# Optimization experiments

Measured on AMD Instinct MI355X. Metric: run time of the kernel, lower is better.

The kernel has to match this reference:

```python
import jax, jax.numpy as jnp
import numpy as np

N, F, M, B = 100000, 256, 10, 32768
DECAY = 0.9


def setup_inputs() -> dict:
    key = jax.random.key(0)
    ks = jax.random.split(key, 16)
    s = 1.0 / np.sqrt(F)
    # forward args
    node_indices = jax.random.permutation(ks[0], N)[:B]  # unique indices
    node_features = jax.random.normal(ks[1], (B, F), jnp.float32)
    # per-node state
    hidden_states = jax.random.normal(ks[2], (N, F), jnp.float32) * 0.1
    cell_states = jax.random.normal(ks[3], (N, F), jnp.float32) * 0.1
    temporal_memory = jax.random.normal(ks[4], (N, M, F), jnp.float32) * 0.1
    memory_ptr = jax.random.randint(ks[5], (N,), 0, M)
    # LSTMCell params (gate order i, f, g, o as in torch)
    W_ih = jax.random.normal(ks[6], (4 * F, F), jnp.float32) * s
    W_hh = jax.random.normal(ks[7], (4 * F, F), jnp.float32) * s
    b_ih = jax.random.normal(ks[8], (4 * F,), jnp.float32) * s
    b_hh = jax.random.normal(ks[9], (4 * F,), jnp.float32) * s
    # attention read params
    Wq = jax.random.normal(ks[10], (F, F), jnp.float32) * s
    bq = jnp.zeros((F,), jnp.float32)
    Wk = jax.random.normal(ks[11], (F, F), jnp.float32) * s
    bk = jnp.zeros((F,), jnp.float32)
    Wv = jax.random.normal(ks[12], (F, F), jnp.float32) * s
    bv = jnp.zeros((F,), jnp.float32)
    return dict(node_indices=node_indices, node_features=node_features,
                hidden_states=hidden_states, cell_states=cell_states,
                temporal_memory=temporal_memory, memory_ptr=memory_ptr,
                W_ih=W_ih, W_hh=W_hh, b_ih=b_ih, b_hh=b_hh,
                Wq=Wq, bq=bq, Wk=Wk, bk=bk, Wv=Wv, bv=bv)


def reference(node_indices, node_features, hidden_states, cell_states,
              temporal_memory, memory_ptr, W_ih, W_hh, b_ih, b_hh,
              Wq, bq, Wk, bk, Wv, bv):
    idx = node_indices
    feat = node_features.shape[-1]
    # --- update_memory: LSTMCell on gathered per-node states ---
    h_prev = hidden_states[idx]              # (B, F)
    c_prev = cell_states[idx]                # (B, F)
    gates = node_features @ W_ih.T + b_ih + h_prev @ W_hh.T + b_hh
    i, f, g, o = jnp.split(gates, 4, axis=-1)
    c_new = jax.nn.sigmoid(f) * c_prev + jax.nn.sigmoid(i) * jnp.tanh(g)
    h_new = jax.nn.sigmoid(o) * jnp.tanh(c_new)
    # --- scatter into circular temporal memory + decay previous slot ---
    ptr = memory_ptr[idx]                    # (B,)
    tm = temporal_memory.at[idx, ptr].set(node_features)
    prev = ptr - 1                           # -1 wraps; decay only applied if ptr > 0
    old = tm[idx, prev]                      # (B, F)
    tm = tm.at[idx, prev].set(jnp.where((ptr > 0)[:, None], old * DECAY, old))
    # --- get_temporal_context: gather + tiny attention over M slots ---
    mem = tm[idx]                            # (B, M, F)
    q = h_new @ Wq.T + bq                    # (B, F)  hidden_states[idx] post-update == h_new
    k = mem @ Wk.T + bk                      # (B, M, F)
    v = mem @ Wv.T + bv                      # (B, M, F)
    scores = jnp.einsum('bf,bmf->bm', q, k) / jnp.sqrt(jnp.asarray(feat, q.dtype))
    w = jax.nn.softmax(scores, axis=-1)      # (B, M)
    context = jnp.einsum('bmf,bm->bf', v, w) # (B, F)
    return context
```

## Files before the change

kernel.cpp:

```cpp
#include <hip/hip_runtime.h>
#include <hip/hip_bf16.h>

constexpr int NB = 32768;
constexpr int NF = 256;
constexpr int NM = 10;
constexpr float DECAY = 0.9f;

using bf16x8 = __attribute__((ext_vector_type(8))) short;
using f32x4  = __attribute__((ext_vector_type(4))) float;

static __device__ __forceinline__ ushort f2bf(float x) {
    unsigned u = __float_as_uint(x);
    unsigned r = (u + 0x7fffu + ((u >> 16) & 1u)) >> 16;
    return (ushort)r;
}
static __device__ __forceinline__ float bf2f(ushort x) {
    return __uint_as_float(((unsigned)x) << 16);
}
static __device__ __forceinline__ float sigmoid_f(float x) {
    return 1.f / (1.f + __expf(-x));
}
static __device__ __forceinline__ float tanh_f(float x) {
    float e = __expf(2.f * x);
    return (e - 1.f) / (e + 1.f);
}
static __device__ __forceinline__ void gload16(const void* g, void* l) {
    __builtin_amdgcn_global_load_lds(
        (const __attribute__((address_space(1))) unsigned int*)g,
        (__attribute__((address_space(3))) unsigned int*)l, 16, 0, 0);
}

constexpr int PB_ACAT = 16384;
constexpr int PB_WGI  = PB_ACAT + 1024;
constexpr int PB_WQKT = PB_WGI + 256;
constexpr int PB_WV   = PB_WQKT + 256;
constexpr int PB_TOT  = PB_WV + 1;

__global__ __launch_bounds__(256) void k_prep(
    const float* __restrict__ W_ih, const float* __restrict__ W_hh,
    const float* __restrict__ b_ih, const float* __restrict__ b_hh,
    const float* __restrict__ Wq, const float* __restrict__ bq,
    const float* __restrict__ Wk, const float* __restrict__ Wv,
    const float* __restrict__ nf, const float* __restrict__ hidden,
    const int* __restrict__ idx,
    ushort* __restrict__ Wgi, float* __restrict__ bsum,
    ushort* __restrict__ WqkT, float* __restrict__ bqk,
    ushort* __restrict__ Wvb, ushort* __restrict__ Acat)
{
    const int blk = blockIdx.x, tid = threadIdx.x;
    if (blk < PB_ACAT) {
        int t = blk * 256 + tid;
        int row = t >> 7;
        int c4 = (t & 127) * 4;
        const float* src = (c4 < 256) ? (nf + (size_t)row * 256 + c4)
                                      : (hidden + (size_t)idx[row] * 256 + (c4 - 256));
        float4 v = *reinterpret_cast<const float4*>(src);
        ushort4 o;
        o.x = f2bf(v.x); o.y = f2bf(v.y); o.z = f2bf(v.z); o.w = f2bf(v.w);
        *reinterpret_cast<ushort4*>(Acat + (size_t)row * 512 + c4) = o;
    } else if (blk < PB_WGI) {
        int j = blk - PB_ACAT;
        int f = j >> 2, g = j & 3;
        int sr = g * 256 + f;
        for (int c = tid; c < 512; c += 256) {
            float v = (c < 256) ? W_ih[sr * 256 + c] : W_hh[sr * 256 + (c - 256)];
            Wgi[j * 512 + c] = f2bf(v);
        }
        if (tid == 0) bsum[j] = b_ih[sr] + b_hh[sr];
    } else if (blk < PB_WQKT) {
        int i = blk - PB_WGI, a = tid;
        float s = 0.f;
#pragma unroll 8
        for (int j = 0; j < 256; ++j) s += Wq[j * 256 + a] * Wk[j * 256 + i];
        WqkT[i * 256 + a] = f2bf(s * 0.0625f);
    } else if (blk < PB_WV) {
        int t = (blk - PB_WQKT) * 256 + tid;
        Wvb[t] = f2bf(Wv[t]);
    } else {
        int i = tid;
        float s = 0.f;
#pragma unroll 8
        for (int j = 0; j < 256; ++j) s += bq[j] * Wk[j * 256 + i];
        bqk[i] = s * 0.0625f;
    }
}

__global__ __launch_bounds__(256) void k_gates2(
    const ushort* __restrict__ Acat, const ushort* __restrict__ Wgi,
    const float* __restrict__ bsum, const int* __restrict__ idx,
    const float* __restrict__ cell, ushort* __restrict__ h_new)
{
    __shared__ ushort As[128 * 32];
    __shared__ ushort Bs[128 * 32];
    const int t = threadIdx.x;
    const int w = t >> 6, l = t & 63;
    const int wr = w >> 1, wc = w & 1;
    const int lr = l & 15, lk = l >> 4;
    const int row0 = blockIdx.x * 128;
    const int col0 = blockIdx.y * 128;

    f32x4 acc[4][4];
#pragma unroll
    for (int m = 0; m < 4; ++m)
#pragma unroll
        for (int n = 0; n < 4; ++n) acc[m][n] = f32x4{0.f, 0.f, 0.f, 0.f};

    const int srow = l >> 2;
    const int scol = (l & 3) * 8;
    const int u0 = w * 2, u1 = u0 + 1;
    const ushort* aS0 = Acat + (size_t)(row0 + u0 * 16 + srow) * 512 + scol;
    const ushort* aS1 = Acat + (size_t)(row0 + u1 * 16 + srow) * 512 + scol;
    const ushort* bS0 = Wgi  + (size_t)(col0 + u0 * 16 + srow) * 512 + scol;
    const ushort* bS1 = Wgi  + (size_t)(col0 + u1 * 16 + srow) * 512 + scol;
    ushort* aL0 = As + u0 * 512; ushort* aL1 = As + u1 * 512;
    ushort* bL0 = Bs + u0 * 512; ushort* bL1 = Bs + u1 * 512;

    for (int k0 = 0; k0 < 512; k0 += 32) {
        gload16(aS0 + k0, aL0);
        gload16(aS1 + k0, aL1);
        gload16(bS0 + k0, bL0);
        gload16(bS1 + k0, bL1);
        __syncthreads();
        bf16x8 af[4], bfr[4];
#pragma unroll
        for (int m = 0; m < 4; ++m)
            af[m] = *reinterpret_cast<const bf16x8*>(As + (wr * 64 + m * 16 + lr) * 32 + lk * 8);
#pragma unroll
        for (int n = 0; n < 4; ++n)
            bfr[n] = *reinterpret_cast<const bf16x8*>(Bs + (wc * 64 + n * 16 + lr) * 32 + lk * 8);
#pragma unroll
        for (int m = 0; m < 4; ++m)
#pragma unroll
            for (int n = 0; n < 4; ++n)
                acc[m][n] = __builtin_amdgcn_mfma_f32_16x16x32_bf16(af[m], bfr[n], acc[m][n], 0, 0, 0);
        __syncthreads();
    }

    float bb[4];
#pragma unroll
    for (int n = 0; n < 4; ++n) bb[n] = bsum[col0 + wc * 64 + n * 16 + lr];
#pragma unroll
    for (int m = 0; m < 4; ++m)
#pragma unroll
        for (int n = 0; n < 4; ++n)
#pragma unroll
            for (int r = 0; r < 4; ++r) acc[m][n][r] += bb[n];

    const int g0 = lr & 3;
    const int fq = lr >> 2;
    const bool is0 = (g0 == 0), is1 = (g0 == 1), is2 = (g0 == 2), is3 = (g0 == 3);
    const int fbase = (col0 >> 2) + wc * 16;

    int nodev[4];
#pragma unroll
    for (int r = 0; r < 4; ++r)
        nodev[r] = idx[row0 + wr * 64 + g0 * 16 + lk * 4 + r];

#pragma unroll
    for (int n = 0; n < 4; ++n) {
#pragma unroll
        for (int r = 0; r < 4; ++r) {
            float own = is0 ? acc[0][n][r] : is1 ? acc[1][n][r] : is2 ? acc[2][n][r] : acc[3][n][r];
            float s1  = is0 ? acc[1][n][r] : is1 ? acc[0][n][r] : is2 ? acc[3][n][r] : acc[2][n][r];
            float s2  = is0 ? acc[2][n][r] : is1 ? acc[3][n][r] : is2 ? acc[0][n][r] : acc[1][n][r];
            float s3  = is0 ? acc[3][n][r] : is1 ? acc[2][n][r] : is2 ? acc[1][n][r] : acc[0][n][r];
            float r1 = __shfl_xor(s1, 1, 64);
            float r2 = __shfl_xor(s2, 2, 64);
            float r3 = __shfl_xor(s3, 3, 64);
            float gi = is0 ? own : is1 ? r1 : is2 ? r2 : r3;
            float gf = is1 ? own : is0 ? r1 : is3 ? r2 : r3;
            float gg = is2 ? own : is3 ? r1 : is0 ? r2 : r3;
            float go = is3 ? own : is2 ? r1 : is1 ? r2 : r3;
            int fg = fbase + n * 4 + fq;
            float cp = cell[(size_t)nodev[r] * 256 + fg];
            float cn = sigmoid_f(gf) * cp + sigmoid_f(gi) * tanh_f(gg);
            float hn = sigmoid_f(go) * tanh_f(cn);
            int grow = row0 + wr * 64 + g0 * 16 + lk * 4 + r;
            h_new[(size_t)grow * 256 + fg] = f2bf(hn);
        }
    }
}

__global__ __launch_bounds__(256) void k_qk(
    const ushort* __restrict__ hnew, const ushort* __restrict__ WqkT,
    const float* __restrict__ bqk, ushort* __restrict__ qbuf)
{
    __shared__ ushort As[64 * 32];
    const int t = threadIdx.x, w = t >> 6, l = t & 63;
    const int lr = l & 15, lk = l >> 4;
    const int row0 = blockIdx.x * 64;

    f32x4 acc[4][4];
#pragma unroll
    for (int m = 0; m < 4; ++m)
#pragma unroll
        for (int n = 0; n < 4; ++n) acc[m][n] = f32x4{0.f, 0.f, 0.f, 0.f};

    const int srow = w * 16 + (l >> 2);
    const int scol = (l & 3) * 8;
    const ushort* aS = hnew + (size_t)(row0 + srow) * 256 + scol;
    ushort* aL = As + (w * 16) * 32;

    const ushort* bptr[4];
#pragma unroll
    for (int n = 0; n < 4; ++n) bptr[n] = WqkT + (size_t)(w * 64 + n * 16 + lr) * 256 + lk * 8;

    for (int k0 = 0; k0 < 256; k0 += 32) {
        gload16(aS + k0, aL);
        __syncthreads();
        bf16x8 a[4], b[4];
#pragma unroll
        for (int m = 0; m < 4; ++m)
            a[m] = *reinterpret_cast<const bf16x8*>(As + (m * 16 + lr) * 32 + lk * 8);
#pragma unroll
        for (int n = 0; n < 4; ++n) b[n] = *reinterpret_cast<const bf16x8*>(bptr[n] + k0);
#pragma unroll
        for (int m = 0; m < 4; ++m)
#pragma unroll
            for (int n = 0; n < 4; ++n)
                acc[m][n] = __builtin_amdgcn_mfma_f32_16x16x32_bf16(a[m], b[n], acc[m][n], 0, 0, 0);
        __syncthreads();
    }

#pragma unroll
    for (int m = 0; m < 4; ++m)
#pragma unroll
        for (int n = 0; n < 4; ++n) {
            int colc = w * 64 + n * 16 + lr;
            float bbq = bqk[colc];
#pragma unroll
            for (int r = 0; r < 4; ++r) {
                int row = row0 + m * 16 + lk * 4 + r;
                qbuf[(size_t)row * 256 + colc] = f2bf(acc[m][n][r] + bbq);
            }
        }
}

static __device__ __forceinline__ int swzb(int row, int byteInRow) {
    return (row * 512 + byteInRow) ^ ((row & 7) << 4);
}

__global__ __launch_bounds__(256) void k_attnout(
    const ushort* __restrict__ qbuf, const ushort* __restrict__ Wvb,
    const float* __restrict__ bv, const int* __restrict__ idx,
    const int* __restrict__ mptr, const float* __restrict__ tm,
    const float* __restrict__ nf, float* __restrict__ out)
{
    __shared__ ushort sQ[16 * 256];
    char* sB = (char*)sQ;
    const int t = threadIdx.x, w = t >> 6, l = t & 63;
    const int lr = l & 15, lk = l >> 4;
    const int row0 = blockIdx.x * 16;

#pragma unroll
    for (int ch = t; ch < 512; ch += 256) {
        int row = ch >> 5;
        int pos = (ch & 31) * 16;
        *reinterpret_cast<uint4*>(sB + swzb(row, pos)) =
            *reinterpret_cast<const uint4*>((const char*)(qbuf + (size_t)(row0 + row) * 256) + pos);
    }
    __syncthreads();

    {
        const int b0 = row0 + w * 4;
        int nodes[4], ptrs[4];
#pragma unroll
        for (int r = 0; r < 4; ++r) { nodes[r] = idx[b0 + r]; ptrs[r] = mptr[nodes[r]]; }

#pragma unroll
        for (int rr = 0; rr < 4; ++rr) {
            int row = w * 4 + rr;
            int b = b0 + rr;
            int node = nodes[rr];
            int ptr = ptrs[rr];
            ushort4 q4 = *(const ushort4*)(sB + swzb(row, l * 8));
            float q0 = bf2f(q4.x), q1 = bf2f(q4.y), q2 = bf2f(q4.z), q3 = bf2f(q4.w);
            const float* base = tm + (size_t)node * (NM * NF);

            float4 mem[NM];
            float sc[NM];
#pragma unroll
            for (int m = 0; m < NM; ++m) {
                float4 v;
                if (m == ptr) {
                    v = *reinterpret_cast<const float4*>(nf + (size_t)b * 256 + l * 4);
                } else {
                    v = *reinterpret_cast<const float4*>(base + (size_t)m * 256 + l * 4);
                    if (ptr > 0 && m == ptr - 1) { v.x *= DECAY; v.y *= DECAY; v.z *= DECAY; v.w *= DECAY; }
                }
                mem[m] = v;
                sc[m] = q0 * v.x + q1 * v.y + q2 * v.z + q3 * v.w;
            }
#pragma unroll
            for (int m = 0; m < NM; ++m) {
                float s = sc[m];
#pragma unroll
                for (int d = 1; d < 64; d <<= 1) s += __shfl_xor(s, d, 64);
                sc[m] = s;
            }
            float mx = sc[0];
#pragma unroll
            for (int m = 1; m < NM; ++m) mx = fmaxf(mx, sc[m]);
            float e[NM], sum = 0.f;
#pragma unroll
            for (int m = 0; m < NM; ++m) { e[m] = __expf(sc[m] - mx); sum += e[m]; }
            float inv = 1.f / sum;

            float4 c = {0.f, 0.f, 0.f, 0.f};
#pragma unroll
            for (int m = 0; m < NM; ++m) {
                float wm = e[m] * inv;
                c.x += wm * mem[m].x; c.y += wm * mem[m].y; c.z += wm * mem[m].z; c.w += wm * mem[m].w;
            }
            ushort4 o;
            o.x = f2bf(c.x); o.y = f2bf(c.y); o.z = f2bf(c.z); o.w = f2bf(c.w);
            *(ushort4*)(sB + swzb(row, l * 8)) = o;
        }
    }
    __syncthreads();

    f32x4 acc[4];
#pragma unroll
    for (int n = 0; n < 4; ++n) acc[n] = f32x4{0.f, 0.f, 0.f, 0.f};
    const ushort* vptr[4];
#pragma unroll
    for (int n = 0; n < 4; ++n) vptr[n] = Wvb + (size_t)(w * 64 + n * 16 + lr) * 256 + lk * 8;

#pragma unroll 2
    for (int k = 0; k < 256; k += 32) {
        bf16x8 a = *reinterpret_cast<const bf16x8*>(sB + swzb(lr, (k + lk * 8) * 2));
        bf16x8 b[4];
#pragma unroll
        for (int n = 0; n < 4; ++n) b[n] = *reinterpret_cast<const bf16x8*>(vptr[n] + k);
#pragma unroll
        for (int n = 0; n < 4; ++n)
            acc[n] = __builtin_amdgcn_mfma_f32_16x16x32_bf16(a, b[n], acc[n], 0, 0, 0);
    }
#pragma unroll
    for (int n = 0; n < 4; ++n) {
        int colc = w * 64 + n * 16 + lr;
        float bbv = bv[colc];
#pragma unroll
        for (int r = 0; r < 4; ++r) {
            int row = lk * 4 + r;
            out[(size_t)(row0 + row) * 256 + colc] = acc[n][r] + bbv;
        }
    }
}

extern "C" void kernel_launch(void* const* d_in, const int* in_sizes, int n_in,
                              void* d_out, int out_size, void* d_ws, size_t ws_size,
                              hipStream_t stream) {
    const int*   node_indices = (const int*)  d_in[0];
    const float* node_feats   = (const float*)d_in[1];
    const float* hidden       = (const float*)d_in[2];
    const float* cell         = (const float*)d_in[3];
    const float* tmem         = (const float*)d_in[4];
    const int*   memory_ptr   = (const int*)  d_in[5];
    const float* W_ih         = (const float*)d_in[6];
    const float* W_hh         = (const float*)d_in[7];
    const float* b_ih         = (const float*)d_in[8];
    const float* b_hh         = (const float*)d_in[9];
    const float* Wq           = (const float*)d_in[10];
    const float* bq           = (const float*)d_in[11];
    const float* Wk           = (const float*)d_in[12];
    const float* Wv           = (const float*)d_in[14];
    const float* bv           = (const float*)d_in[15];

    char* ws = (char*)d_ws;
    size_t off = 0;
    auto alloc = [&](size_t bytes) { char* p = ws + off; off += (bytes + 255) & ~(size_t)255; return p; };

    ushort* Wgi   = (ushort*)alloc((size_t)1024 * 512 * 2);
    ushort* WqkT  = (ushort*)alloc((size_t)256 * 256 * 2);
    ushort* Wvb   = (ushort*)alloc((size_t)256 * 256 * 2);
    float*  bqk   = (float*) alloc((size_t)256 * 4);
    float*  bsum  = (float*) alloc((size_t)1024 * 4);
    ushort* Acat  = (ushort*)alloc((size_t)NB * 512 * 2);
    ushort* hnew  = (ushort*)alloc((size_t)NB * 256 * 2);
    ushort* qbuf  = (ushort*)alloc((size_t)NB * 256 * 2);

    k_prep<<<PB_TOT, 256, 0, stream>>>(W_ih, W_hh, b_ih, b_hh, Wq, bq, Wk, Wv,
                                       node_feats, hidden, node_indices,
                                       Wgi, bsum, WqkT, bqk, Wvb, Acat);
    k_gates2<<<dim3(NB / 128, 8), 256, 0, stream>>>(Acat, Wgi, bsum, node_indices, cell, hnew);
    k_qk<<<NB / 64, 256, 0, stream>>>(hnew, WqkT, bqk, qbuf);
    k_attnout<<<NB / 16, 256, 0, stream>>>(qbuf, Wvb, bv, node_indices, memory_ptr,
                                           tmem, node_feats, (float*)d_out);
}
```

Measured before the change: 218.8 us.

## Double-buffer LDS tiles in GEMM kernels and read q directly from global

The gates and qk GEMM kernels now double-buffer their shared-memory A/B tiles, prefetching the next K-slice while MFMAs consume the current one. This halves the barriers per iteration and overlaps global loads with compute. The attention-output kernel drops its staging of q into swizzled LDS and loads each row's q values directly from global memory. The cost is twice the shared memory in the GEMMs, which may reduce occupancy.

```diff
diff --git a/kernel.cpp b/kernel.cpp
--- a/kernel.cpp
+++ b/kernel.cpp
@@ -90,8 +90,8 @@
     const float* __restrict__ bsum, const int* __restrict__ idx,
     const float* __restrict__ cell, ushort* __restrict__ h_new)
 {
-    __shared__ ushort As[128 * 32];
-    __shared__ ushort Bs[128 * 32];
+    __shared__ ushort As[2][128 * 32];
+    __shared__ ushort Bs[2][128 * 32];
     const int t = threadIdx.x;
     const int w = t >> 6, l = t & 63;
     const int wr = w >> 1, wc = w & 1;
@@ -112,28 +112,35 @@
     const ushort* aS1 = Acat + (size_t)(row0 + u1 * 16 + srow) * 512 + scol;
     const ushort* bS0 = Wgi  + (size_t)(col0 + u0 * 16 + srow) * 512 + scol;
     const ushort* bS1 = Wgi  + (size_t)(col0 + u1 * 16 + srow) * 512 + scol;
-    ushort* aL0 = As + u0 * 512; ushort* aL1 = As + u1 * 512;
-    ushort* bL0 = Bs + u0 * 512; ushort* bL1 = Bs + u1 * 512;
+
+    gload16(aS0, As[0] + u0 * 512);
+    gload16(aS1, As[0] + u1 * 512);
+    gload16(bS0, Bs[0] + u0 * 512);
+    gload16(bS1, Bs[0] + u1 * 512);
+    __syncthreads();
 
     for (int k0 = 0; k0 < 512; k0 += 32) {
-        gload16(aS0 + k0, aL0);
-        gload16(aS1 + k0, aL1);
-        gload16(bS0 + k0, bL0);
-        gload16(bS1 + k0, bL1);
-        __syncthreads();
+        const int cur = (k0 >> 5) & 1;
+        if (k0 + 32 < 512) {
+            const int nxt = cur ^ 1;
+            gload16(aS0 + k0 + 32, As[nxt] + u0 * 512);
+            gload16(aS1 + k0 + 32, As[nxt] + u1 * 512);
+            gload16(bS0 + k0 + 32, Bs[nxt] + u0 * 512);
+            gload16(bS1 + k0 + 32, Bs[nxt] + u1 * 512);
+        }
         bf16x8 af[4], bfr[4];
 #pragma unroll
         for (int m = 0; m < 4; ++m)
-            af[m] = *reinterpret_cast<const bf16x8*>(As + (wr * 64 + m * 16 + lr) * 32 + lk * 8);
+            af[m] = *reinterpret_cast<const bf16x8*>(As[cur] + (wr * 64 + m * 16 + lr) * 32 + lk * 8);
 #pragma unroll
         for (int n = 0; n < 4; ++n)
-            bfr[n] = *reinterpret_cast<const bf16x8*>(Bs + (wc * 64 + n * 16 + lr) * 32 + lk * 8);
+            bfr[n] = *reinterpret_cast<const bf16x8*>(Bs[cur] + (wc * 64 + n * 16 + lr) * 32 + lk * 8);
 #pragma unroll
         for (int m = 0; m < 4; ++m)
 #pragma unroll
             for (int n = 0; n < 4; ++n)
                 acc[m][n] = __builtin_amdgcn_mfma_f32_16x16x32_bf16(af[m], bfr[n], acc[m][n], 0, 0, 0);
-        __syncthreads();
+        if (k0 + 32 < 512) __syncthreads();
     }
 
     float bb[4];
@@ -185,7 +192,7 @@
     const ushort* __restrict__ hnew, const ushort* __restrict__ WqkT,
     const float* __restrict__ bqk, ushort* __restrict__ qbuf)
 {
-    __shared__ ushort As[64 * 32];
+    __shared__ ushort As[2][64 * 32];
     const int t = threadIdx.x, w = t >> 6, l = t & 63;
     const int lr = l & 15, lk = l >> 4;
     const int row0 = blockIdx.x * 64;
@@ -199,19 +206,22 @@
     const int srow = w * 16 + (l >> 2);
     const int scol = (l & 3) * 8;
     const ushort* aS = hnew + (size_t)(row0 + srow) * 256 + scol;
-    ushort* aL = As + (w * 16) * 32;
+    const int aLoff = (w * 16) * 32;
 
     const ushort* bptr[4];
 #pragma unroll
     for (int n = 0; n < 4; ++n) bptr[n] = WqkT + (size_t)(w * 64 + n * 16 + lr) * 256 + lk * 8;
 
+    gload16(aS, As[0] + aLoff);
+    __syncthreads();
+
     for (int k0 = 0; k0 < 256; k0 += 32) {
-        gload16(aS + k0, aL);
-        __syncthreads();
+        const int cur = (k0 >> 5) & 1;
+        if (k0 + 32 < 256) gload16(aS + k0 + 32, As[cur ^ 1] + aLoff);
         bf16x8 a[4], b[4];
 #pragma unroll
         for (int m = 0; m < 4; ++m)
-            a[m] = *reinterpret_cast<const bf16x8*>(As + (m * 16 + lr) * 32 + lk * 8);
+            a[m] = *reinterpret_cast<const bf16x8*>(As[cur] + (m * 16 + lr) * 32 + lk * 8);
 #pragma unroll
         for (int n = 0; n < 4; ++n) b[n] = *reinterpret_cast<const bf16x8*>(bptr[n] + k0);
 #pragma unroll
@@ -219,7 +229,7 @@
 #pragma unroll
             for (int n = 0; n < 4; ++n)
                 acc[m][n] = __builtin_amdgcn_mfma_f32_16x16x32_bf16(a[m], b[n], acc[m][n], 0, 0, 0);
-        __syncthreads();
+        if (k0 + 32 < 256) __syncthreads();
     }
 
 #pragma unroll
@@ -246,20 +256,11 @@
     const int* __restrict__ mptr, const float* __restrict__ tm,
     const float* __restrict__ nf, float* __restrict__ out)
 {
-    __shared__ ushort sQ[16 * 256];
-    char* sB = (char*)sQ;
+    __shared__ ushort sC[16 * 256];
+    char* sB = (char*)sC;
     const int t = threadIdx.x, w = t >> 6, l = t & 63;
     const int lr = l & 15, lk = l >> 4;
     const int row0 = blockIdx.x * 16;
-
-#pragma unroll
-    for (int ch = t; ch < 512; ch += 256) {
-        int row = ch >> 5;
-        int pos = (ch & 31) * 16;
-        *reinterpret_cast<uint4*>(sB + swzb(row, pos)) =
-            *reinterpret_cast<const uint4*>((const char*)(qbuf + (size_t)(row0 + row) * 256) + pos);
-    }
-    __syncthreads();
 
     {
         const int b0 = row0 + w * 4;
@@ -273,7 +274,7 @@
             int b = b0 + rr;
             int node = nodes[rr];
             int ptr = ptrs[rr];
-            ushort4 q4 = *(const ushort4*)(sB + swzb(row, l * 8));
+            ushort4 q4 = *reinterpret_cast<const ushort4*>(qbuf + (size_t)b * 256 + l * 4);
             float q0 = bf2f(q4.x), q1 = bf2f(q4.y), q2 = bf2f(q4.z), q3 = bf2f(q4.w);
             const float* base = tm + (size_t)node * (NM * NF);
 
```

Result: slower. 228.4 us (+4.4%).

## Fuse Q projection into attention kernel and pipeline gates with tail in quarters

Applied to the files above, without the earlier changes.

Folds the q projection (h_new·WqkT) into the attention/output kernel, so q stays in shared memory and the qbuf global round trip disappears. The batch is split into four quarters. Mixed launches run the gates GEMM for quarter q alongside the tail for quarter q-1 in one grid, so compute-heavy and memory-heavy blocks overlap. The cost is more launches, a larger shared footprint on mixed blocks, and tail blocks that now compute q for 16 rows, each reloading the full WqkT.

```diff
diff --git a/kernel.cpp b/kernel.cpp
--- a/kernel.cpp
+++ b/kernel.cpp
@@ -28,6 +28,9 @@
     __builtin_amdgcn_global_load_lds(
         (const __attribute__((address_space(1))) unsigned int*)g,
         (__attribute__((address_space(3))) unsigned int*)l, 16, 0, 0);
+}
+static __device__ __forceinline__ int swzb(int row, int byteInRow) {
+    return (row * 512 + byteInRow) ^ ((row & 7) << 4);
 }
 
 constexpr int PB_ACAT = 16384;
@@ -85,19 +88,20 @@
     }
 }
 
-__global__ __launch_bounds__(256) void k_gates2(
+__device__ __forceinline__ void gates_body(
+    char* smem, int bx, int by, int qg,
     const ushort* __restrict__ Acat, const ushort* __restrict__ Wgi,
     const float* __restrict__ bsum, const int* __restrict__ idx,
     const float* __restrict__ cell, ushort* __restrict__ h_new)
 {
-    __shared__ ushort As[128 * 32];
-    __shared__ ushort Bs[128 * 32];
+    ushort* As = (ushort*)smem;
+    ushort* Bs = (ushort*)(smem + 8192);
     const int t = threadIdx.x;
     const int w = t >> 6, l = t & 63;
     const int wr = w >> 1, wc = w & 1;
     const int lr = l & 15, lk = l >> 4;
-    const int row0 = blockIdx.x * 128;
-    const int col0 = blockIdx.y * 128;
+    const int row0 = (qg * 64 + bx) * 128;
+    const int col0 = by * 128;
 
     f32x4 acc[4][4];
 #pragma unroll
@@ -181,83 +185,47 @@
     }
 }
 
-__global__ __launch_bounds__(256) void k_qk(
+__device__ __forceinline__ void tail_body(
+    char* smem, int tb, int qt,
     const ushort* __restrict__ hnew, const ushort* __restrict__ WqkT,
-    const float* __restrict__ bqk, ushort* __restrict__ qbuf)
-{
-    __shared__ ushort As[64 * 32];
+    const float* __restrict__ bqk, const ushort* __restrict__ Wvb,
+    const float* __restrict__ bv, const int* __restrict__ idx,
+    const int* __restrict__ mptr, const float* __restrict__ tm,
+    const float* __restrict__ nf, float* __restrict__ out)
+{
+    char* sB = smem;
     const int t = threadIdx.x, w = t >> 6, l = t & 63;
     const int lr = l & 15, lk = l >> 4;
-    const int row0 = blockIdx.x * 64;
-
-    f32x4 acc[4][4];
-#pragma unroll
-    for (int m = 0; m < 4; ++m)
-#pragma unroll
-        for (int n = 0; n < 4; ++n) acc[m][n] = f32x4{0.f, 0.f, 0.f, 0.f};
-
-    const int srow = w * 16 + (l >> 2);
-    const int scol = (l & 3) * 8;
-    const ushort* aS = hnew + (size_t)(row0 + srow) * 256 + scol;
-    ushort* aL = As + (w * 16) * 32;
-
-    const ushort* bptr[4];
-#pragma unroll
-    for (int n = 0; n < 4; ++n) bptr[n] = WqkT + (size_t)(w * 64 + n * 16 + lr) * 256 + lk * 8;
-
-    for (int k0 = 0; k0 < 256; k0 += 32) {
-        gload16(aS + k0, aL);
-        __syncthreads();
-        bf16x8 a[4], b[4];
-#pragma unroll
-        for (int m = 0; m < 4; ++m)
-            a[m] = *reinterpret_cast<const bf16x8*>(As + (m * 16 + lr) * 32 + lk * 8);
-#pragma unroll
-        for (int n = 0; n < 4; ++n) b[n] = *reinterpret_cast<const bf16x8*>(bptr[n] + k0);
-#pragma unroll
-        for (int m = 0; m < 4; ++m)
+    const int row0 = (qt * 512 + tb) * 16;
+
+    {
+        f32x4 qa[4];
+#pragma unroll
+        for (int n = 0; n < 4; ++n) qa[n] = f32x4{0.f, 0.f, 0.f, 0.f};
+        const ushort* ap = hnew + (size_t)(row0 + lr) * 256 + lk * 8;
+        const ushort* bp[4];
+#pragma unroll
+        for (int n = 0; n < 4; ++n) bp[n] = WqkT + (size_t)(w * 64 + n * 16 + lr) * 256 + lk * 8;
+#pragma unroll 2
+        for (int k0 = 0; k0 < 256; k0 += 32) {
+            bf16x8 a = *reinterpret_cast<const bf16x8*>(ap + k0);
+            bf16x8 b[4];
+#pragma unroll
+            for (int n = 0; n < 4; ++n) b[n] = *reinterpret_cast<const bf16x8*>(bp[n] + k0);
 #pragma unroll
             for (int n = 0; n < 4; ++n)
-                acc[m][n] = __builtin_amdgcn_mfma_f32_16x16x32_bf16(a[m], b[n], acc[m][n], 0, 0, 0);
-        __syncthreads();
-    }
-
-#pragma unroll
-    for (int m = 0; m < 4; ++m)
+                qa[n] = __builtin_amdgcn_mfma_f32_16x16x32_bf16(a, b[n], qa[n], 0, 0, 0);
+        }
 #pragma unroll
         for (int n = 0; n < 4; ++n) {
             int colc = w * 64 + n * 16 + lr;
             float bbq = bqk[colc];
 #pragma unroll
             for (int r = 0; r < 4; ++r) {
-                int row = row0 + m * 16 + lk * 4 + r;
-                qbuf[(size_t)row * 256 + colc] = f2bf(acc[m][n][r] + bbq);
+                int row = lk * 4 + r;
+                *(ushort*)(sB + swzb(row, colc * 2)) = f2bf(qa[n][r] + bbq);
             }
         }
-}
-
-static __device__ __forceinline__ int swzb(int row, int byteInRow) {
-    return (row * 512 + byteInRow) ^ ((row & 7) << 4);
-}
-
-__global__ __launch_bounds__(256) void k_attnout(
-    const ushort* __restrict__ qbuf, const ushort* __restrict__ Wvb,
-    const float* __restrict__ bv, const int* __restrict__ idx,
-    const int* __restrict__ mptr, const float* __restrict__ tm,
-    const float* __restrict__ nf, float* __restrict__ out)
-{
-    __shared__ ushort sQ[16 * 256];
-    char* sB = (char*)sQ;
-    const int t = threadIdx.x, w = t >> 6, l = t & 63;
-    const int lr = l & 15, lk = l >> 4;
-    const int row0 = blockIdx.x * 16;
-
-#pragma unroll
-    for (int ch = t; ch < 512; ch += 256) {
-        int row = ch >> 5;
-        int pos = (ch & 31) * 16;
-        *reinterpret_cast<uint4*>(sB + swzb(row, pos)) =
-            *reinterpret_cast<const uint4*>((const char*)(qbuf + (size_t)(row0 + row) * 256) + pos);
     }
     __syncthreads();
 
@@ -319,32 +287,75 @@
     }
     __syncthreads();
 
-    f32x4 acc[4];
-#pragma unroll
-    for (int n = 0; n < 4; ++n) acc[n] = f32x4{0.f, 0.f, 0.f, 0.f};
-    const ushort* vptr[4];
-#pragma unroll
-    for (int n = 0; n < 4; ++n) vptr[n] = Wvb + (size_t)(w * 64 + n * 16 + lr) * 256 + lk * 8;
+    {
+        f32x4 acc[4];
+#pragma unroll
+        for (int n = 0; n < 4; ++n) acc[n] = f32x4{0.f, 0.f, 0.f, 0.f};
+        const ushort* vptr[4];
+#pragma unroll
+        for (int n = 0; n < 4; ++n) vptr[n] = Wvb + (size_t)(w * 64 + n * 16 + lr) * 256 + lk * 8;
 
 #pragma unroll 2
-    for (int k = 0; k < 256; k += 32) {
-        bf16x8 a = *reinterpret_cast<const bf16x8*>(sB + swzb(lr, (k + lk * 8) * 2));
-        bf16x8 b[4];
-#pragma unroll
-        for (int n = 0; n < 4; ++n) b[n] = *reinterpret_cast<const bf16x8*>(vptr[n] + k);
-#pragma unroll
-        for (int n = 0; n < 4; ++n)
-            acc[n] = __builtin_amdgcn_mfma_f32_16x16x32_bf16(a, b[n], acc[n], 0, 0, 0);
-    }
-#pragma unroll
-    for (int n = 0; n < 4; ++n) {
-        int colc = w * 64 + n * 16 + lr;
-        float bbv = bv[colc];
-#pragma unroll
-        for (int r = 0; r < 4; ++r) {
-            int row = lk * 4 + r;
-            out[(size_t)(row0 + row) * 256 + colc] = acc[n][r] + bbv;
-        }
+        for (int k = 0; k < 256; k += 32) {
+            bf16x8 a = *reinterpret_cast<const bf16x8*>(sB + swzb(lr, (k + lk * 8) * 2));
+            bf16x8 b[4];
+#pragma unroll
+            for (int n = 0; n < 4; ++n) b[n] = *reinterpret_cast<const bf16x8*>(vptr[n] + k);
+#pragma unroll
+            for (int n = 0; n < 4; ++n)
+                acc[n] = __builtin_amdgcn_mfma_f32_16x16x32_bf16(a, b[n], acc[n], 0, 0, 0);
+        }
+#pragma unroll
+        for (int n = 0; n < 4; ++n) {
+            int colc = w * 64 + n * 16 + lr;
+            float bbv = bv[colc];
+#pragma unroll
+            for (int r = 0; r < 4; ++r) {
+                int row = lk * 4 + r;
+                out[(size_t)(row0 + row) * 256 + colc] = acc[n][r] + bbv;
+            }
+        }
+    }
+}
+
+__global__ __launch_bounds__(256) void k_gatesQ(
+    int qg,
+    const ushort* __restrict__ Acat, const ushort* __restrict__ Wgi,
+    const float* __restrict__ bsum, const int* __restrict__ idx,
+    const float* __restrict__ cell, ushort* __restrict__ h_new)
+{
+    __shared__ char smem[16384];
+    gates_body(smem, blockIdx.x, blockIdx.y, qg, Acat, Wgi, bsum, idx, cell, h_new);
+}
+
+__global__ __launch_bounds__(256) void k_tailQ(
+    int qt,
+    const ushort* __restrict__ hnew, const ushort* __restrict__ WqkT,
+    const float* __restrict__ bqk, const ushort* __restrict__ Wvb,
+    const float* __restrict__ bv, const int* __restrict__ idx,
+    const int* __restrict__ mptr, const float* __restrict__ tm,
+    const float* __restrict__ nf, float* __restrict__ out)
+{
+    __shared__ char smem[8192];
+    tail_body(smem, blockIdx.x, qt, hnew, WqkT, bqk, Wvb, bv, idx, mptr, tm, nf, out);
+}
+
+__global__ __launch_bounds__(256) void k_mix(
+    int qg, int qt,
+    const ushort* __restrict__ Acat, const ushort* __restrict__ Wgi,
+    const float* __restrict__ bsum, const int* __restrict__ idx,
+    const float* __restrict__ cell, ushort* __restrict__ h_new,
+    const ushort* __restrict__ WqkT, const float* __restrict__ bqk,
+    const ushort* __restrict__ Wvb, const float* __restrict__ bv,
+    const int* __restrict__ mptr, const float* __restrict__ tm,
+    const float* __restrict__ nf, float* __restrict__ out)
+{
+    __shared__ char smem[16384];
+    if (blockIdx.x < 512) {
+        tail_body(smem, blockIdx.x, qt, h_new, WqkT, bqk, Wvb, bv, idx, mptr, tm, nf, out);
+    } else {
+        int bi = blockIdx.x - 512;
+        gates_body(smem, bi & 63, bi >> 6, qg, Acat, Wgi, bsum, idx, cell, h_new);
     }
 }
 
@@ -378,13 +389,16 @@
     float*  bsum  = (float*) alloc((size_t)1024 * 4);
     ushort* Acat  = (ushort*)alloc((size_t)NB * 512 * 2);
     ushort* hnew  = (ushort*)alloc((size_t)NB * 256 * 2);
-    ushort* qbuf  = (ushort*)alloc((size_t)NB * 256 * 2);
 
     k_prep<<<PB_TOT, 256, 0, stream>>>(W_ih, W_hh, b_ih, b_hh, Wq, bq, Wk, Wv,
                                        node_feats, hidden, node_indices,
                                        Wgi, bsum, WqkT, bqk, Wvb, Acat);
-    k_gates2<<<dim3(NB / 128, 8), 256, 0, stream>>>(Acat, Wgi, bsum, node_indices, cell, hnew);
-    k_qk<<<NB / 64, 256, 0, stream>>>(hnew, WqkT, bqk, qbuf);
-    k_attnout<<<NB / 16, 256, 0, stream>>>(qbuf, Wvb, bv, node_indices, memory_ptr,
-                                           tmem, node_feats, (float*)d_out);
-}
+    k_gatesQ<<<dim3(64, 8), 256, 0, stream>>>(0, Acat, Wgi, bsum, node_indices, cell, hnew);
+    for (int q = 1; q < 4; ++q) {
+        k_mix<<<1024, 256, 0, stream>>>(q, q - 1, Acat, Wgi, bsum, node_indices, cell, hnew,
+                                        WqkT, bqk, Wvb, bv, memory_ptr, tmem, node_feats,
+                                        (float*)d_out);
+    }
+    k_tailQ<<<512, 256, 0, stream>>>(3, hnew, WqkT, bqk, Wvb, bv, node_indices, memory_ptr,
+                                     tmem, node_feats, (float*)d_out);
+}
```

Result: slower. 258.1 us (+17.9%).
